# Optimization experiments

Measured on AMD Instinct MI355X. Metric: run time of the kernel, lower is better.

The kernel has to match this reference:

```python
import jax, jax.numpy as jnp
import numpy as np
from math import sqrt

B, L, S, H, E, D = 4, 2048, 2048, 16, 64, 64


def setup_inputs() -> dict:
    key = jax.random.key(0)
    kq, kk, kv = jax.random.split(key, 3)
    queries = jax.random.normal(kq, (B, L, H, E), dtype=jnp.float32)
    keys = jax.random.normal(kk, (B, S, H, E), dtype=jnp.float32)
    values = jax.random.normal(kv, (B, S, H, D), dtype=jnp.float32)
    # TriangularCausalMask: True above the diagonal (positions to mask out)
    attn_mask = jnp.broadcast_to(
        jnp.triu(jnp.ones((L, S), dtype=bool), k=1)[None, None], (B, 1, L, S)
    )
    return {"queries": queries, "keys": keys, "values": values, "attn_mask": attn_mask}


def reference(queries, keys, values, attn_mask):
    # B, L, H, E = queries.shape ; scale = 1/sqrt(E) (self.scale is None)
    scale = 1.0 / sqrt(queries.shape[-1])
    # scores: [B, H, L, S]
    scores = jnp.einsum("blhe,bshe->bhls", queries, keys)
    # mask_flag=True: masked_fill with -inf before scaling (scale*(-inf) = -inf)
    scores = jnp.where(attn_mask, -jnp.inf, scores)
    A = jax.nn.softmax(scale * scores, axis=-1)  # dropout p=0.0 -> identity
    V = jnp.einsum("bhls,bshd->blhd", A, values)
    return V
```

## Files before the change

kernel.cpp:

```cpp
#include <hip/hip_runtime.h>
#include <hip/hip_bf16.h>

typedef __bf16 bf16x8 __attribute__((ext_vector_type(8)));
typedef float floatx4 __attribute__((ext_vector_type(4)));
typedef unsigned int u32;

#define Bc 4
#define Lc 2048
#define Sc 2048
#define Hc 16
#define Ec 64
#define Dc 64
#define NQT (Lc/64)
#define NPAIR (NQT/2)
#define NT (Sc/64)
#define TILEB 8192
#define WSK ((size_t)Bc*Hc*NT*TILEB)
#define WSNEED (2*WSK)

__device__ __forceinline__ bf16x8 pack8f(const float* f){
  bf16x8 r;
  #pragma unroll
  for (int i=0;i<8;++i) r[i] = (__bf16)f[i];
  return r;
}

template<int CTRL>
__device__ __forceinline__ float dppf(float x){
  return __builtin_bit_cast(float,
    __builtin_amdgcn_update_dpp(0, __builtin_bit_cast(int, x), CTRL, 0xF, 0xF, true));
}
__device__ __forceinline__ float rowmax16(float x){
  x = fmaxf(x, dppf<0xB1>(x));
  x = fmaxf(x, dppf<0x4E>(x));
  x = fmaxf(x, dppf<0x141>(x));
  x = fmaxf(x, dppf<0x140>(x));
  return x;
}
__device__ __forceinline__ float rowsum16(float x){
  x += dppf<0xB1>(x);
  x += dppf<0x4E>(x);
  x += dppf<0x141>(x);
  x += dppf<0x140>(x);
  return x;
}

__device__ __forceinline__ void gload16(const void* g, void* l){
  __builtin_amdgcn_global_load_lds(
      (const __attribute__((address_space(1))) u32*)g,
      (__attribute__((address_space(3))) u32*)l, 16, 0, 0);
}

__global__ __launch_bounds__(256)
void prep(const float* __restrict__ K, const float* __restrict__ V,
          char* __restrict__ ws)
{
  const int t = blockIdx.x*256 + threadIdx.x;
  if (t < (1<<20)) {
    const int c = t & 7, r = (t>>3) & 63, tile = (t>>9) & 31, h = (t>>14) & 15, b = t>>18;
    const float* src = K + ((size_t)((b*Sc + tile*64 + r))*Hc + h)*Ec + c*8;
    float tmp[8];
    *(float4*)(tmp)   = *(const float4*)(src);
    *(float4*)(tmp+4) = *(const float4*)(src + 4);
    char* dst = ws + (size_t)((b*Hc + h)*NT + tile)*TILEB + r*128 + ((c ^ (r&7))<<4);
    *(bf16x8*)dst = pack8f(tmp);
  } else {
    const int u = t - (1<<20);
    const int d = u & 63, c = (u>>6) & 7, tile = (u>>9) & 31, h = (u>>14) & 15, b = u>>18;
    const float* src = V + ((size_t)((b*Sc + tile*64 + c*8))*Hc + h)*Dc + d;
    bf16x8 v;
    #pragma unroll
    for (int kk=0; kk<8; ++kk) v[kk] = (__bf16)src[(size_t)kk*Hc*Dc];
    char* dst = ws + WSK + (size_t)((b*Hc + h)*NT + tile)*TILEB + d*128 + ((c ^ (d&7))<<4);
    *(bf16x8*)dst = v;
  }
}

__global__ __launch_bounds__(256)
void fa_fwd(const float* __restrict__ Q, const char* __restrict__ ws,
            float* __restrict__ O)
{
  int nid = blockIdx.x;
  int bid = (nid & 7) * ((int)gridDim.x >> 3) + (nid >> 3);
  int pid = bid & (NPAIR - 1);
  int h  = (bid >> 4) & (Hc - 1);
  int b  = bid >> 8;

  int tid  = threadIdx.x;
  int w    = tid >> 6;
  int lane = tid & 63;
  int lg   = lane >> 4;
  int lr   = lane & 15;

  __shared__ __align__(16) char Kl[2][64*128];
  __shared__ __align__(16) char Vl[2][64*128];
  __shared__ __align__(16) char Pl[4][16*64*2];
  char* Pw = Pl[w];

  const char* gK = ws +        (size_t)((b*Hc + h)*NT)*TILEB;
  const char* gV = ws + WSK +  (size_t)((b*Hc + h)*NT)*TILEB;
  const int soff = w*2048 + lane*16;

  #pragma unroll 1
  for (int pass=0; pass<2; ++pass) {
    const int qt = pass ? (NQT-1-pid) : pid;

    const int qrow = qt*64 + w*16 + lr;
    const float* qp = Q + ((size_t)(b*Lc + qrow)*Hc + h)*Ec;
    bf16x8 aq[2];
    {
      float tmp[8];
      #pragma unroll
      for (int c=0; c<2; ++c) {
        *(float4*)(tmp)   = *(const float4*)(qp + c*32 + lg*8);
        *(float4*)(tmp+4) = *(const float4*)(qp + c*32 + lg*8 + 4);
        #pragma unroll
        for (int i=0;i<8;++i) tmp[i] *= 0.125f;
        aq[c] = pack8f(tmp);
      }
    }

    floatx4 o[4];
    float m[4], lsum[4];
    #pragma unroll
    for (int i=0;i<4;++i){ o[i] = (floatx4){0.f,0.f,0.f,0.f}; m[i] = -3.0e38f; lsum[i] = 0.f; }

    {
      const char* sK = gK + soff;
      const char* sV = gV + soff;
      gload16(sK,        &Kl[0][w*2048]);
      gload16(sK + 1024, &Kl[0][w*2048 + 1024]);
      gload16(sV,        &Vl[0][w*2048]);
      gload16(sV + 1024, &Vl[0][w*2048 + 1024]);
    }
    __syncthreads();

    const int nt = qt + 1;
    for (int t = 0; t < nt; ++t) {
      char* Kcur = Kl[t&1];
      char* Vcur = Vl[t&1];

      if (t+1 < nt) {
        const int nb = (t+1)&1;
        const char* sK = gK + (size_t)(t+1)*TILEB + soff;
        const char* sV = gV + (size_t)(t+1)*TILEB + soff;
        gload16(sK,        &Kl[nb][w*2048]);
        gload16(sK + 1024, &Kl[nb][w*2048 + 1024]);
        gload16(sV,        &Vl[nb][w*2048]);
        gload16(sV + 1024, &Vl[nb][w*2048 + 1024]);
      }

      floatx4 s[4];
      #pragma unroll
      for (int nf=0; nf<4; ++nf) {
        int kr = nf*16 + lr;
        unsigned xr = (kr & 7) << 4;
        const char* kp = Kcur + kr*128;
        bf16x8 b0 = *(const bf16x8*)(kp + ((lg*16)      ^ xr));
        bf16x8 b1 = *(const bf16x8*)(kp + ((64 + lg*16) ^ xr));
        floatx4 acc = (floatx4){0.f,0.f,0.f,0.f};
        acc = __builtin_amdgcn_mfma_f32_16x16x32_bf16(aq[0], b0, acc, 0, 0, 0);
        acc = __builtin_amdgcn_mfma_f32_16x16x32_bf16(aq[1], b1, acc, 0, 0, 0);
        s[nf] = acc;
      }

      if (t == qt) {
        #pragma unroll
        for (int nf=0; nf<4; ++nf)
          #pragma unroll
          for (int r=0; r<4; ++r)
            if (nf*16 + lr > w*16 + lg*4 + r) s[nf][r] = -3.0e38f;
      }

      float mx[4], rs[4], al[4];
      #pragma unroll
      for (int r=0;r<4;++r) {
        mx[r] = rowmax16(fmaxf(fmaxf(s[0][r], s[1][r]), fmaxf(s[2][r], s[3][r])));
        float mn = fmaxf(m[r], mx[r]);
        al[r] = __expf(m[r] - mn);
        m[r] = mn;
        rs[r] = 0.f;
      }
      #pragma unroll
      for (int nf=0; nf<4; ++nf)
        #pragma unroll
        for (int r=0;r<4;++r) {
          float p = __expf(s[nf][r] - m[r]);
          rs[r] += p;
          s[nf][r] = p;
        }
      #pragma unroll
      for (int r=0;r<4;++r) {
        rs[r] = rowsum16(rs[r]);
        lsum[r] = lsum[r]*al[r] + rs[r];
      }
      #pragma unroll
      for (int df=0; df<4; ++df)
        #pragma unroll
        for (int r=0;r<4;++r) o[df][r] *= al[r];

      #pragma unroll
      for (int nf=0; nf<4; ++nf)
        #pragma unroll
        for (int r=0;r<4;++r) {
          int q = lg*4 + r;
          int k = nf*16 + lr;
          *(__bf16*)(Pw + q*128 + ((k*2) ^ ((q&7)<<4))) = (__bf16)s[nf][r];
        }

      {
        unsigned xq = (lr & 7) << 4;
        const char* pp = Pw + lr*128;
        bf16x8 pa0 = *(const bf16x8*)(pp + ((lg*16)      ^ xq));
        bf16x8 pa1 = *(const bf16x8*)(pp + ((64 + lg*16) ^ xq));
        #pragma unroll
        for (int df=0; df<4; ++df) {
          int d = df*16 + lr;
          unsigned xd = (d & 7) << 4;
          const char* vp = Vcur + d*128;
          bf16x8 vb0 = *(const bf16x8*)(vp + ((lg*16)      ^ xd));
          bf16x8 vb1 = *(const bf16x8*)(vp + ((64 + lg*16) ^ xd));
          o[df] = __builtin_amdgcn_mfma_f32_16x16x32_bf16(pa0, vb0, o[df], 0, 0, 0);
          o[df] = __builtin_amdgcn_mfma_f32_16x16x32_bf16(pa1, vb1, o[df], 0, 0, 0);
        }
      }
      __syncthreads();
    }

    #pragma unroll
    for (int r=0;r<4;++r) {
      float inv = 1.0f / lsum[r];
      int qg = qt*64 + w*16 + lg*4 + r;
      float* op = O + ((size_t)(b*Lc + qg)*Hc + h)*Dc;
      #pragma unroll
      for (int df=0; df<4; ++df)
        op[df*16 + lr] = o[df][r] * inv;
    }
  }
}

#define QB 128
#define NQTB (Lc/QB)
#define NPAIRB (NQTB/2)

__global__ __launch_bounds__(256)
void fa_fwd_fb(const float* __restrict__ Q, const float* __restrict__ K,
               const float* __restrict__ V, float* __restrict__ O)
{
  int nid = blockIdx.x;
  int bid = (nid & 7) * ((int)gridDim.x >> 3) + (nid >> 3);
  int pid = bid & (NPAIRB - 1);
  int h  = (bid >> 3) & (Hc - 1);
  int b  = bid >> 7;

  int tid  = threadIdx.x;
  int w    = tid >> 6;
  int lane = tid & 63;
  int lg   = lane >> 4;
  int lr   = lane & 15;

  __shared__ __align__(16) char Kl[2][64*128];
  __shared__ __align__(16) char Vl[2][64*128];
  __shared__ __align__(16) char Pl[4][16*64*2];
  char* Pw = Pl[w];

  const int skr = tid >> 2, seg = tid & 3;
  const int sd  = tid & 63, skb = tid >> 6;
  const unsigned xk = (skr & 7) << 4;
  const unsigned xv = (sd  & 7) << 4;

  const float* Kb = K + ((size_t)(b*Sc)*Hc + h)*Ec;
  const float* Vb = V + ((size_t)(b*Sc)*Hc + h)*Dc;

  float kf[16], vf[16];

  #pragma unroll 1
  for (int pass=0; pass<2; ++pass) {
    const int qtb = pass ? (NQTB-1-pid) : pid;
    const int q0w = qtb*QB + w*32;

    bf16x8 aq[2][2];
    #pragma unroll
    for (int s2=0; s2<2; ++s2) {
      const float* qp = Q + ((size_t)(b*Lc + q0w + s2*16 + lr)*Hc + h)*Ec;
      float tmp[8];
      #pragma unroll
      for (int c=0; c<2; ++c) {
        *(float4*)(tmp)   = *(const float4*)(qp + c*32 + lg*8);
        *(float4*)(tmp+4) = *(const float4*)(qp + c*32 + lg*8 + 4);
        #pragma unroll
        for (int i=0;i<8;++i) tmp[i] *= 0.125f;
        aq[s2][c] = pack8f(tmp);
      }
    }

    floatx4 o[2][4];
    float m[2][4], lsum[2][4];
    #pragma unroll
    for (int s2=0; s2<2; ++s2)
      #pragma unroll
      for (int i=0;i<4;++i){ o[s2][i] = (floatx4){0.f,0.f,0.f,0.f}; m[s2][i] = -3.0e38f; lsum[s2][i] = 0.f; }

    {
      const float* ks = Kb + (size_t)skr*Hc*Ec + seg*16;
      *(float4*)(kf)    = *(const float4*)(ks);
      *(float4*)(kf+4)  = *(const float4*)(ks+4);
      *(float4*)(kf+8)  = *(const float4*)(ks+8);
      *(float4*)(kf+12) = *(const float4*)(ks+12);
      const float* vs = Vb + (size_t)(skb*16)*Hc*Dc + sd;
      #pragma unroll
      for (int i=0;i<16;++i) vf[i] = vs[(size_t)i*Hc*Dc];
    }

    const int nt = 2*qtb + 2;
    for (int t = 0; t < nt; ++t) {
      char* Kcur = Kl[t&1];
      char* Vcur = Vl[t&1];

      *(bf16x8*)(Kcur + skr*128 + ((seg*32)      ^ xk)) = pack8f(kf);
      *(bf16x8*)(Kcur + skr*128 + ((seg*32 + 16) ^ xk)) = pack8f(kf+8);
      *(bf16x8*)(Vcur + sd*128  + ((skb*32)      ^ xv)) = pack8f(vf);
      *(bf16x8*)(Vcur + sd*128  + ((skb*32 + 16) ^ xv)) = pack8f(vf+8);
      __syncthreads();

      if (t+1 < nt) {
        const float* ks = Kb + (size_t)((t+1)*64 + skr)*Hc*Ec + seg*16;
        *(float4*)(kf)    = *(const float4*)(ks);
        *(float4*)(kf+4)  = *(const float4*)(ks+4);
        *(float4*)(kf+8)  = *(const float4*)(ks+8);
        *(float4*)(kf+12) = *(const float4*)(ks+12);
        const float* vs = Vb + (size_t)((t+1)*64 + skb*16)*Hc*Dc + sd;
        #pragma unroll
        for (int i=0;i<16;++i) vf[i] = vs[(size_t)i*Hc*Dc];
      }

      if (t*64 <= q0w + 31) {
        const int t64 = t*64;
        const bool needmask = (t64 + 63 > q0w);

        #pragma unroll
        for (int s2=0; s2<2; ++s2) {
          floatx4 s[4];
          #pragma unroll
          for (int nf=0; nf<4; ++nf) {
            int kr = nf*16 + lr;
            unsigned xr = (kr & 7) << 4;
            const char* kp = Kcur + kr*128;
            bf16x8 b0 = *(const bf16x8*)(kp + ((lg*16)      ^ xr));
            bf16x8 b1 = *(const bf16x8*)(kp + ((64 + lg*16) ^ xr));
            floatx4 acc = (floatx4){0.f,0.f,0.f,0.f};
            acc = __builtin_amdgcn_mfma_f32_16x16x32_bf16(aq[s2][0], b0, acc, 0, 0, 0);
            acc = __builtin_amdgcn_mfma_f32_16x16x32_bf16(aq[s2][1], b1, acc, 0, 0, 0);
            s[nf] = acc;
          }

          if (needmask) {
            const int qq = q0w + s2*16 + lg*4;
            #pragma unroll
            for (int nf=0; nf<4; ++nf)
              #pragma unroll
              for (int r=0; r<4; ++r)
                if (t64 + nf*16 + lr > qq + r) s[nf][r] = -3.0e38f;
          }

          float mx[4], rs[4], al[4];
          #pragma unroll
          for (int r=0;r<4;++r) {
            mx[r] = rowmax16(fmaxf(fmaxf(s[0][r], s[1][r]), fmaxf(s[2][r], s[3][r])));
            float mn = fmaxf(m[s2][r], mx[r]);
            al[r] = __expf(m[s2][r] - mn);
            m[s2][r] = mn;
            rs[r] = 0.f;
          }
          #pragma unroll
          for (int nf=0; nf<4; ++nf)
            #pragma unroll
            for (int r=0;r<4;++r) {
              float p = __expf(s[nf][r] - m[s2][r]);
              rs[r] += p;
              s[nf][r] = p;
            }
          #pragma unroll
          for (int r=0;r<4;++r) {
            rs[r] = rowsum16(rs[r]);
            lsum[s2][r] = lsum[s2][r]*al[r] + rs[r];
          }
          #pragma unroll
          for (int df=0; df<4; ++df)
            #pragma unroll
            for (int r=0;r<4;++r) o[s2][df][r] *= al[r];

          #pragma unroll
          for (int nf=0; nf<4; ++nf)
            #pragma unroll
            for (int r=0;r<4;++r) {
              int q = lg*4 + r;
              int k = nf*16 + lr;
              *(__bf16*)(Pw + q*128 + ((k*2) ^ ((q&7)<<4))) = (__bf16)s[nf][r];
            }

          {
            unsigned xq = (lr & 7) << 4;
            const char* pp = Pw + lr*128;
            bf16x8 pa0 = *(const bf16x8*)(pp + ((lg*16)      ^ xq));
            bf16x8 pa1 = *(const bf16x8*)(pp + ((64 + lg*16) ^ xq));
            #pragma unroll
            for (int df=0; df<4; ++df) {
              int d = df*16 + lr;
              unsigned xd = (d & 7) << 4;
              const char* vp = Vcur + d*128;
              bf16x8 vb0 = *(const bf16x8*)(vp + ((lg*16)      ^ xd));
              bf16x8 vb1 = *(const bf16x8*)(vp + ((64 + lg*16) ^ xd));
              o[s2][df] = __builtin_amdgcn_mfma_f32_16x16x32_bf16(pa0, vb0, o[s2][df], 0, 0, 0);
              o[s2][df] = __builtin_amdgcn_mfma_f32_16x16x32_bf16(pa1, vb1, o[s2][df], 0, 0, 0);
            }
          }
        }
      }
      __syncthreads();
    }

    #pragma unroll
    for (int s2=0; s2<2; ++s2)
      #pragma unroll
      for (int r=0;r<4;++r) {
        float inv = 1.0f / lsum[s2][r];
        int qg = q0w + s2*16 + lg*4 + r;
        float* op = O + ((size_t)(b*Lc + qg)*Hc + h)*Dc;
        #pragma unroll
        for (int df=0; df<4; ++df)
          op[df*16 + lr] = o[s2][df][r] * inv;
      }
  }
}

extern "C" void kernel_launch(void* const* d_in, const int* in_sizes, int n_in,
                              void* d_out, int out_size, void* d_ws, size_t ws_size,
                              hipStream_t stream) {
  const float* Q = (const float*)d_in[0];
  const float* K = (const float*)d_in[1];
  const float* V = (const float*)d_in[2];
  float* O = (float*)d_out;

  if (ws_size >= WSNEED) {
    char* ws = (char*)d_ws;
    prep<<<dim3((2u<<20)/256), dim3(256), 0, stream>>>(K, V, ws);
    fa_fwd<<<dim3(Bc * Hc * NPAIR), dim3(256), 0, stream>>>(Q, ws, O);
  } else {
    fa_fwd_fb<<<dim3(Bc * Hc * NPAIRB), dim3(256), 0, stream>>>(Q, K, V, O);
  }
}
```

Measured before the change: 111.7 us.

## Halve KV tile to 32 keys, skip masked warps, lazily rescale softmax

Splits each 64-key tile into two 32-key subtiles with a new swizzled V staging layout, so warps whose rows sit entirely above the diagonal skip the QK and PV work for a subtile. It folds log2(e) into the Q scale so it can use exp2f, and rescales the running max, sum and output only when some row's max grows past a threshold. This is aimed at cutting wasted causal-diagonal work and exp/rescale instructions. The cost is twice as many loop iterations and barriers, plus extra control flow.

```diff
diff --git a/kernel.cpp b/kernel.cpp
--- a/kernel.cpp
+++ b/kernel.cpp
@@ -17,6 +17,8 @@
 #define TILEB 8192
 #define WSK ((size_t)Bc*Hc*NT*TILEB)
 #define WSNEED (2*WSK)
+#define QSC 0.18033688011112042f
+#define THR 11.5f
 
 __device__ __forceinline__ bf16x8 pack8f(const float* f){
   bf16x8 r;
@@ -92,14 +94,20 @@
   int lg   = lane >> 4;
   int lr   = lane & 15;
 
-  __shared__ __align__(16) char Kl[2][64*128];
-  __shared__ __align__(16) char Vl[2][64*128];
+  __shared__ __align__(16) char Kl[2][32*128];
+  __shared__ __align__(16) char Vl[2][64*64];
   __shared__ __align__(16) char Pl[4][16*64*2];
   char* Pw = Pl[w];
 
   const char* gK = ws +        (size_t)((b*Hc + h)*NT)*TILEB;
   const char* gV = ws + WSK +  (size_t)((b*Hc + h)*NT)*TILEB;
-  const int soff = w*2048 + lane*16;
+
+  const int dL = w*16 + (lane>>2);
+  const int pL = lane & 3;
+  const int cl = pL ^ ((dL>>2)&3);
+  const int vo0 = dL*128 + ((( cl    ) ^ (dL&7))<<4);
+  const int vo1 = dL*128 + ((( cl + 4) ^ (dL&7))<<4);
+  const int kso = w*1024 + lane*16;
 
   #pragma unroll 1
   for (int pass=0; pass<2; ++pass) {
@@ -115,7 +123,7 @@
         *(float4*)(tmp)   = *(const float4*)(qp + c*32 + lg*8);
         *(float4*)(tmp+4) = *(const float4*)(qp + c*32 + lg*8 + 4);
         #pragma unroll
-        for (int i=0;i<8;++i) tmp[i] *= 0.125f;
+        for (int i=0;i<8;++i) tmp[i] *= QSC;
         aq[c] = pack8f(tmp);
       }
     }
@@ -125,103 +133,96 @@
     #pragma unroll
     for (int i=0;i<4;++i){ o[i] = (floatx4){0.f,0.f,0.f,0.f}; m[i] = -3.0e38f; lsum[i] = 0.f; }
 
-    {
-      const char* sK = gK + soff;
-      const char* sV = gV + soff;
-      gload16(sK,        &Kl[0][w*2048]);
-      gload16(sK + 1024, &Kl[0][w*2048 + 1024]);
-      gload16(sV,        &Vl[0][w*2048]);
-      gload16(sV + 1024, &Vl[0][w*2048 + 1024]);
-    }
+    gload16(gK + kso, &Kl[0][w*1024]);
+    gload16(gV + vo0, &Vl[0][w*1024]);
     __syncthreads();
 
-    const int nt = qt + 1;
+    const int nt = 2*qt + 2;
     for (int t = 0; t < nt; ++t) {
       char* Kcur = Kl[t&1];
       char* Vcur = Vl[t&1];
 
       if (t+1 < nt) {
         const int nb = (t+1)&1;
-        const char* sK = gK + (size_t)(t+1)*TILEB + soff;
-        const char* sV = gV + (size_t)(t+1)*TILEB + soff;
-        gload16(sK,        &Kl[nb][w*2048]);
-        gload16(sK + 1024, &Kl[nb][w*2048 + 1024]);
-        gload16(sV,        &Vl[nb][w*2048]);
-        gload16(sV + 1024, &Vl[nb][w*2048 + 1024]);
-      }
-
-      floatx4 s[4];
-      #pragma unroll
-      for (int nf=0; nf<4; ++nf) {
-        int kr = nf*16 + lr;
-        unsigned xr = (kr & 7) << 4;
-        const char* kp = Kcur + kr*128;
-        bf16x8 b0 = *(const bf16x8*)(kp + ((lg*16)      ^ xr));
-        bf16x8 b1 = *(const bf16x8*)(kp + ((64 + lg*16) ^ xr));
-        floatx4 acc = (floatx4){0.f,0.f,0.f,0.f};
-        acc = __builtin_amdgcn_mfma_f32_16x16x32_bf16(aq[0], b0, acc, 0, 0, 0);
-        acc = __builtin_amdgcn_mfma_f32_16x16x32_bf16(aq[1], b1, acc, 0, 0, 0);
-        s[nf] = acc;
-      }
-
-      if (t == qt) {
-        #pragma unroll
-        for (int nf=0; nf<4; ++nf)
-          #pragma unroll
-          for (int r=0; r<4; ++r)
-            if (nf*16 + lr > w*16 + lg*4 + r) s[nf][r] = -3.0e38f;
-      }
-
-      float mx[4], rs[4], al[4];
-      #pragma unroll
-      for (int r=0;r<4;++r) {
-        mx[r] = rowmax16(fmaxf(fmaxf(s[0][r], s[1][r]), fmaxf(s[2][r], s[3][r])));
-        float mn = fmaxf(m[r], mx[r]);
-        al[r] = __expf(m[r] - mn);
-        m[r] = mn;
-        rs[r] = 0.f;
-      }
-      #pragma unroll
-      for (int nf=0; nf<4; ++nf)
+        const int t1 = t+1;
+        gload16(gK + (size_t)t1*4096 + kso, &Kl[nb][w*1024]);
+        gload16(gV + (size_t)(t1>>1)*TILEB + ((t1&1) ? vo1 : vo0), &Vl[nb][w*1024]);
+      }
+
+      const int kbase = t*32 - qt*64;
+      if (kbase <= w*16 + 15) {
+
+        floatx4 s[2];
+        #pragma unroll
+        for (int nf=0; nf<2; ++nf) {
+          int kr = nf*16 + lr;
+          unsigned xr = (kr & 7) << 4;
+          const char* kp = Kcur + kr*128;
+          bf16x8 b0 = *(const bf16x8*)(kp + ((lg*16)      ^ xr));
+          bf16x8 b1 = *(const bf16x8*)(kp + ((64 + lg*16) ^ xr));
+          floatx4 acc = (floatx4){0.f,0.f,0.f,0.f};
+          acc = __builtin_amdgcn_mfma_f32_16x16x32_bf16(aq[0], b0, acc, 0, 0, 0);
+          acc = __builtin_amdgcn_mfma_f32_16x16x32_bf16(aq[1], b1, acc, 0, 0, 0);
+          s[nf] = acc;
+        }
+
+        if (kbase + 31 > w*16) {
+          #pragma unroll
+          for (int nf=0; nf<2; ++nf)
+            #pragma unroll
+            for (int r=0; r<4; ++r)
+              if (kbase + nf*16 + lr > w*16 + lg*4 + r) s[nf][r] = -3.0e38f;
+        }
+
+        float mx[4];
+        float need = -1.f;
         #pragma unroll
         for (int r=0;r<4;++r) {
-          float p = __expf(s[nf][r] - m[r]);
-          rs[r] += p;
-          s[nf][r] = p;
-        }
-      #pragma unroll
-      for (int r=0;r<4;++r) {
-        rs[r] = rowsum16(rs[r]);
-        lsum[r] = lsum[r]*al[r] + rs[r];
-      }
-      #pragma unroll
-      for (int df=0; df<4; ++df)
-        #pragma unroll
-        for (int r=0;r<4;++r) o[df][r] *= al[r];
-
-      #pragma unroll
-      for (int nf=0; nf<4; ++nf)
-        #pragma unroll
-        for (int r=0;r<4;++r) {
-          int q = lg*4 + r;
-          int k = nf*16 + lr;
-          *(__bf16*)(Pw + q*128 + ((k*2) ^ ((q&7)<<4))) = (__bf16)s[nf][r];
-        }
-
-      {
-        unsigned xq = (lr & 7) << 4;
-        const char* pp = Pw + lr*128;
-        bf16x8 pa0 = *(const bf16x8*)(pp + ((lg*16)      ^ xq));
-        bf16x8 pa1 = *(const bf16x8*)(pp + ((64 + lg*16) ^ xq));
-        #pragma unroll
-        for (int df=0; df<4; ++df) {
-          int d = df*16 + lr;
-          unsigned xd = (d & 7) << 4;
-          const char* vp = Vcur + d*128;
-          bf16x8 vb0 = *(const bf16x8*)(vp + ((lg*16)      ^ xd));
-          bf16x8 vb1 = *(const bf16x8*)(vp + ((64 + lg*16) ^ xd));
-          o[df] = __builtin_amdgcn_mfma_f32_16x16x32_bf16(pa0, vb0, o[df], 0, 0, 0);
-          o[df] = __builtin_amdgcn_mfma_f32_16x16x32_bf16(pa1, vb1, o[df], 0, 0, 0);
+          mx[r] = rowmax16(fmaxf(s[0][r], s[1][r]));
+          need = fmaxf(need, mx[r] - m[r]);
+        }
+        if (__any(need > THR)) {
+          #pragma unroll
+          for (int r=0;r<4;++r) {
+            float mn = fmaxf(m[r], mx[r]);
+            float al = exp2f(m[r] - mn);
+            m[r] = mn;
+            lsum[r] *= al;
+            #pragma unroll
+            for (int df=0; df<4; ++df) o[df][r] *= al;
+          }
+        }
+
+        float rs[4] = {0.f,0.f,0.f,0.f};
+        #pragma unroll
+        for (int nf=0; nf<2; ++nf)
+          #pragma unroll
+          for (int r=0;r<4;++r) {
+            float p = exp2f(s[nf][r] - m[r]);
+            rs[r] += p;
+            s[nf][r] = p;
+          }
+        #pragma unroll
+        for (int r=0;r<4;++r) lsum[r] += rowsum16(rs[r]);
+
+        #pragma unroll
+        for (int nf=0; nf<2; ++nf)
+          #pragma unroll
+          for (int r=0;r<4;++r) {
+            int q = lg*4 + r;
+            int k = nf*16 + lr;
+            *(__bf16*)(Pw + q*128 + ((k*2) ^ ((q&7)<<4))) = (__bf16)s[nf][r];
+          }
+
+        {
+          unsigned xq = (lr & 7) << 4;
+          bf16x8 pa = *(const bf16x8*)(Pw + lr*128 + ((lg*16) ^ xq));
+          #pragma unroll
+          for (int df=0; df<4; ++df) {
+            int d = df*16 + lr;
+            bf16x8 vb = *(const bf16x8*)(Vcur + d*64 + ((lg ^ ((d>>2)&3))<<4));
+            o[df] = __builtin_amdgcn_mfma_f32_16x16x32_bf16(pa, vb, o[df], 0, 0, 0);
+          }
         }
       }
       __syncthreads();
```

Measured after the change: 149.7 us. +34.0%, slower.
